# Optimization experiments

Hardware: AMD Instinct MI355X
Metric: run time of the kernel (lower is better)

Reference implementation:

```python
import jax, jax.numpy as jnp
import numpy as np

N_NODES = 100000


def _gcn_conv(x, edge_index, W, b, n_nodes):
    # GCNConv: add self-loops, symmetric degree normalization, then
    # out[dst] += norm * (x @ W)[src], plus bias.
    src, dst = edge_index[0], edge_index[1]
    loops = jnp.arange(n_nodes, dtype=src.dtype)
    src = jnp.concatenate([src, loops])
    dst = jnp.concatenate([dst, loops])
    deg = jax.ops.segment_sum(jnp.ones_like(dst, dtype=x.dtype), dst,
                              num_segments=n_nodes)
    dinv = jnp.where(deg > 0, jax.lax.rsqrt(deg), 0.0)
    norm = dinv[src] * dinv[dst]            # [E+N]
    h = x @ W                               # [N, out]  (transform BEFORE gather)
    msg = h[src] * norm[:, None]            # [E+N, out]
    out = jax.ops.segment_sum(msg, dst, num_segments=n_nodes)
    return out + b


def setup_inputs() -> dict:
    key = jax.random.key(0)
    ks = jax.random.split(key, 5)
    x = jax.random.normal(ks[0], (N_NODES, 512), dtype=jnp.float32)
    edge_index = jax.random.randint(ks[1], (2, 3200000), 0, N_NODES, dtype=jnp.int64)
    W1 = jax.random.normal(ks[2], (512, 16), dtype=jnp.float32) * (1.0 / np.sqrt(512))
    b1 = jnp.zeros((16,), dtype=jnp.float32)
    W2 = jax.random.normal(ks[3], (16, 7), dtype=jnp.float32) * (1.0 / np.sqrt(16))
    b2 = jnp.zeros((7,), dtype=jnp.float32)
    return {"x": x, "edge_index": edge_index, "W1": W1, "b1": b1, "W2": W2, "b2": b2}


def reference(x, edge_index, W1, b1, W2, b2):
    n = x.shape[0]
    h = _gcn_conv(x, edge_index, W1, b1, n)
    h = jax.nn.relu(h)
    # F.dropout(training=False) is identity in eval mode
    h = _gcn_conv(h, edge_index, W2, b2, n)
    return jax.nn.log_softmax(h, axis=1)
```

## Files before the change

### kernel.cpp

```cpp
#include <hip/hip_runtime.h>
#include <hip/hip_bf16.h>

#define N_NODES 100000
#define N_EDGES 3200000
#define F_IN    512
#define F_H     16
#define F_OUT   7
#define NB      391
#define GPART   512
#define PER_BLK 6256
#define NTILES  6250
#define CAPB    10240

typedef unsigned int u32;
typedef __attribute__((ext_vector_type(8))) __bf16 bf16x8;
typedef __attribute__((ext_vector_type(4))) float f32x4;

union FragU { uint4 q; bf16x8 v; };

static __device__ __forceinline__ float bflo(u32 u) { return __uint_as_float(u << 16); }
static __device__ __forceinline__ float bfhi(u32 u) { return __uint_as_float(u & 0xFFFF0000u); }
static __device__ __forceinline__ unsigned short f2bf(float f) {
  u32 x = __float_as_uint(f);
  x += 0x7FFF + ((x >> 16) & 1);
  return (unsigned short)(x >> 16);
}
static __device__ __forceinline__ u32 cvt2(float a, float b) {
  u32 r;
  asm("v_cvt_pk_bf16_f32 %0, %1, %2" : "=v"(r) : "v"(a), "v"(b));
  return r;
}

__global__ __launch_bounds__(256) void k_hist(const int* __restrict__ dst,
                                              int* __restrict__ hist,
                                              int* __restrict__ bcnt) {
  __shared__ int h[NB];
  int tid = threadIdx.x, blk = blockIdx.x;
  for (int b = tid; b < NB; b += 256) h[b] = 0;
  __syncthreads();
  int e0 = blk * PER_BLK;
  int n = min(PER_BLK, N_EDGES - e0);
  const int4* d4 = (const int4*)(dst + e0);
  for (int i = tid; i < (n >> 2); i += 256) {
    int4 d = d4[i];
    atomicAdd(&h[d.x >> 8], 1);
    atomicAdd(&h[d.y >> 8], 1);
    atomicAdd(&h[d.z >> 8], 1);
    atomicAdd(&h[d.w >> 8], 1);
  }
  __syncthreads();
  for (int b = tid; b < NB; b += 256) {
    int c = h[b];
    hist[blk * NB + b] = c;
    if (c) atomicAdd(&bcnt[b], c);
  }
}

__global__ __launch_bounds__(512) void k_scanprep(const int* __restrict__ bcnt,
                                                  int* __restrict__ pbase,
                                                  int* __restrict__ gcur,
                                                  const float* __restrict__ W1,
                                                  uint4* __restrict__ bfragG) {
  int tid = threadIdx.x;
  if (blockIdx.x == 1) {
    for (int idx = tid; idx < 1024; idx += 512) {
      int kk = idx >> 6, lane = idx & 63;
      int col = lane & 15, g = lane >> 4;
      int k0 = kk * 32 + g * 8;
      uint4 q;
      q.x = cvt2(W1[(k0 + 0) * 16 + col], W1[(k0 + 1) * 16 + col]);
      q.y = cvt2(W1[(k0 + 2) * 16 + col], W1[(k0 + 3) * 16 + col]);
      q.z = cvt2(W1[(k0 + 4) * 16 + col], W1[(k0 + 5) * 16 + col]);
      q.w = cvt2(W1[(k0 + 6) * 16 + col], W1[(k0 + 7) * 16 + col]);
      bfragG[idx] = q;
    }
    return;
  }
  __shared__ int lds[512];
  int c = (tid < NB) ? bcnt[tid] : 0;
  lds[tid] = c;
  __syncthreads();
  for (int off = 1; off < 512; off <<= 1) {
    int v = (tid >= off) ? lds[tid - off] : 0;
    __syncthreads();
    lds[tid] += v;
    __syncthreads();
  }
  int ex = lds[tid] - c;
  if (tid <= NB) pbase[tid] = ex;
  if (tid < NB) gcur[tid] = ex;
}

__global__ __launch_bounds__(256) void k_part(const int* __restrict__ src,
                                              const int* __restrict__ dst,
                                              const int* __restrict__ hist,
                                              int* __restrict__ gcur,
                                              u32* __restrict__ pairs) {
  __shared__ int lbase[NB];
  __shared__ int lcur[NB];
  int tid = threadIdx.x, blk = blockIdx.x;
  for (int b = tid; b < NB; b += 256) {
    int c = hist[blk * NB + b];
    lbase[b] = c ? atomicAdd(&gcur[b], c) : 0;
    lcur[b] = 0;
  }
  __syncthreads();
  int e0 = blk * PER_BLK;
  int n = min(PER_BLK, N_EDGES - e0);
  const int4* s4 = (const int4*)(src + e0);
  const int4* d4 = (const int4*)(dst + e0);
  for (int i = tid; i < (n >> 2); i += 256) {
    int4 sv = s4[i];
    int4 dv = d4[i];
    { int b = dv.x >> 8; u32 v = ((u32)(dv.x & 255) << 17) | (u32)sv.x;
      pairs[lbase[b] + atomicAdd(&lcur[b], 1)] = v; }
    { int b = dv.y >> 8; u32 v = ((u32)(dv.y & 255) << 17) | (u32)sv.y;
      pairs[lbase[b] + atomicAdd(&lcur[b], 1)] = v; }
    { int b = dv.z >> 8; u32 v = ((u32)(dv.z & 255) << 17) | (u32)sv.z;
      pairs[lbase[b] + atomicAdd(&lcur[b], 1)] = v; }
    { int b = dv.w >> 8; u32 v = ((u32)(dv.w & 255) << 17) | (u32)sv.w;
      pairs[lbase[b] + atomicAdd(&lcur[b], 1)] = v; }
  }
}

__global__ __launch_bounds__(256) void k_deg(const u32* __restrict__ pairs,
                                             const int* __restrict__ pbase,
                                             int* __restrict__ deg) {
  __shared__ int h[256];
  int tid = threadIdx.x, b = blockIdx.x;
  h[tid] = 0;
  __syncthreads();
  int base = pbase[b], cnt = pbase[b + 1] - base;
  for (int k = tid; k < cnt; k += 256)
    atomicAdd(&h[pairs[base + k] >> 17], 1);
  __syncthreads();
  int node = b * 256 + tid;
  if (node < N_NODES) deg[node] = h[tid];
}

__global__ __launch_bounds__(256) void k_gemm1(const float* __restrict__ x,
                                               const uint4* __restrict__ bfragG,
                                               const int* __restrict__ deg,
                                               unsigned short* __restrict__ h1p) {
  __shared__ __align__(16) char ldsbuf[2][64 * 80];
  int tid = threadIdx.x;
  int blockRow0 = blockIdx.x * 64;

  int r0 = tid >> 3, r1 = r0 + 32, s = tid & 7;
  bool ok1 = (blockRow0 + r1) < N_NODES;
  const float* x0 = x + (size_t)(blockRow0 + r0) * F_IN + s * 4;
  const float* x1 = x + (size_t)(blockRow0 + r1) * F_IN + s * 4;

  int wv = tid >> 6, lane = tid & 63;
  int col = lane & 15, g = lane >> 4;
  int wid = blockIdx.x * 4 + wv;
  int fragRow = wv * 16 + col;

  f32x4 acc = {0.f, 0.f, 0.f, 0.f};

  {
    float4 fA = *(const float4*)(x0);
    float4 fB = ok1 ? *(const float4*)(x1) : make_float4(0.f, 0.f, 0.f, 0.f);
    uint2 qA = {cvt2(fA.x, fA.y), cvt2(fA.z, fA.w)};
    uint2 qB = {cvt2(fB.x, fB.y), cvt2(fB.z, fB.w)};
    *(uint2*)(&ldsbuf[0][r0 * 80 + s * 8]) = qA;
    *(uint2*)(&ldsbuf[0][r1 * 80 + s * 8]) = qB;
  }
  __syncthreads();

#pragma unroll
  for (int kk = 0; kk < 16; kk++) {
    int cur = kk & 1;
    float4 fA, fB;
    if (kk < 15) {
      fA = *(const float4*)(x0 + (kk + 1) * 32);
      fB = ok1 ? *(const float4*)(x1 + (kk + 1) * 32) : make_float4(0.f, 0.f, 0.f, 0.f);
    }
    FragU a, b;
    a.q = *(const uint4*)(&ldsbuf[cur][fragRow * 80 + g * 16]);
    b.q = bfragG[kk * 64 + lane];
    acc = __builtin_amdgcn_mfma_f32_16x16x32_bf16(a.v, b.v, acc, 0, 0, 0);
    if (kk < 15) {
      uint2 qA = {cvt2(fA.x, fA.y), cvt2(fA.z, fA.w)};
      uint2 qB = {cvt2(fB.x, fB.y), cvt2(fB.z, fB.w)};
      *(uint2*)(&ldsbuf[cur ^ 1][r0 * 80 + s * 8]) = qA;
      *(uint2*)(&ldsbuf[cur ^ 1][r1 * 80 + s * 8]) = qB;
    }
    __syncthreads();
  }

#pragma unroll
  for (int r = 0; r < 4; r++) {
    int node = wid * 16 + g * 4 + r;
    if (node < N_NODES) {
      float di = rsqrtf((float)(deg[node] + 1));
      h1p[(size_t)node * F_H + col] = f2bf(di * acc[r]);
    }
  }
}

__global__ __launch_bounds__(512) void k_agg1(const u32* __restrict__ pairs,
                                              const int* __restrict__ pbase,
                                              const unsigned short* __restrict__ h1p,
                                              const float* __restrict__ b1,
                                              const float* __restrict__ W2,
                                              unsigned short* __restrict__ gfp) {
  __shared__ u32 col[CAPB];
  __shared__ int hist256[256];
  __shared__ int scan_[256];
  __shared__ int excl[256];
  __shared__ int cur[256];
  int tid = threadIdx.x, b = blockIdx.x;
  if (tid < 256) { hist256[tid] = 0; cur[tid] = 0; }
  __syncthreads();
  int base = pbase[b], cnt = pbase[b + 1] - base;
  for (int k = tid; k < cnt; k += 512)
    atomicAdd(&hist256[pairs[base + k] >> 17], 1);
  __syncthreads();
  if (tid < 256) scan_[tid] = hist256[tid];
  __syncthreads();
  for (int off = 1; off < 256; off <<= 1) {
    int v = 0;
    if (tid < 256 && tid >= off) v = scan_[tid - off];
    __syncthreads();
    if (tid < 256) scan_[tid] += v;
    __syncthreads();
  }
  if (tid < 256) excl[tid] = scan_[tid] - hist256[tid];
  __syncthreads();
  for (int k = tid; k < cnt; k += 512) {
    u32 v = pairs[base + k];
    int dl = v >> 17;
    col[excl[dl] + atomicAdd(&cur[dl], 1)] = v & 0x1FFFF;
  }
  __syncthreads();

  int dl = tid >> 1, h = tid & 1;
  int node = b * 256 + dl;
  if (node >= N_NODES) return;
  int s0 = excl[dl], c0 = hist256[dl];
  const uint4* hp = (const uint4*)h1p;
  float a[8] = {0.f, 0.f, 0.f, 0.f, 0.f, 0.f, 0.f, 0.f};
  for (int e = s0; e < s0 + c0; e++) {
    uint4 hv = hp[col[e] * 2 + h];
    a[0] += bflo(hv.x); a[1] += bfhi(hv.x);
    a[2] += bflo(hv.y); a[3] += bfhi(hv.y);
    a[4] += bflo(hv.z); a[5] += bfhi(hv.z);
    a[6] += bflo(hv.w); a[7] += bfhi(hv.w);
  }
  {
    uint4 hv = hp[node * 2 + h];
    a[0] += bflo(hv.x); a[1] += bfhi(hv.x);
    a[2] += bflo(hv.y); a[3] += bfhi(hv.y);
    a[4] += bflo(hv.z); a[5] += bfhi(hv.z);
    a[6] += bflo(hv.w); a[7] += bfhi(hv.w);
  }
  float di = rsqrtf((float)(c0 + 1));
  float own[8];
#pragma unroll
  for (int k = 0; k < 8; k++)
    own[k] = fmaxf(di * a[k] + b1[h * 8 + k], 0.f);
  float oth[8];
#pragma unroll
  for (int k = 0; k < 8; k++) oth[k] = __shfl_xor(own[k], 1, 64);
  if (h == 0) {
    float o[7] = {0.f, 0.f, 0.f, 0.f, 0.f, 0.f, 0.f};
#pragma unroll
    for (int k = 0; k < 8; k++)
#pragma unroll
      for (int j = 0; j < 7; j++)
        o[j] += own[k] * W2[k * 7 + j] + oth[k] * W2[(k + 8) * 7 + j];
    uint4 q;
    q.x = cvt2(di * o[0], di * o[1]);
    q.y = cvt2(di * o[2], di * o[3]);
    q.z = cvt2(di * o[4], di * o[5]);
    q.w = cvt2(di * o[6], 0.f);
    ((uint4*)gfp)[node] = q;
  }
}

__global__ __launch_bounds__(512) void k_agg2(const u32* __restrict__ pairs,
                                              const int* __restrict__ pbase,
                                              const unsigned short* __restrict__ gfp,
                                              const float* __restrict__ b2,
                                              float* __restrict__ out) {
  __shared__ u32 col[CAPB];
  __shared__ int hist256[256];
  __shared__ int scan_[256];
  __shared__ int excl[256];
  __shared__ int cur[256];
  int tid = threadIdx.x, b = blockIdx.x;
  if (tid < 256) { hist256[tid] = 0; cur[tid] = 0; }
  __syncthreads();
  int base = pbase[b], cnt = pbase[b + 1] - base;
  for (int k = tid; k < cnt; k += 512)
    atomicAdd(&hist256[pairs[base + k] >> 17], 1);
  __syncthreads();
  if (tid < 256) scan_[tid] = hist256[tid];
  __syncthreads();
  for (int off = 1; off < 256; off <<= 1) {
    int v = 0;
    if (tid < 256 && tid >= off) v = scan_[tid - off];
    __syncthreads();
    if (tid < 256) scan_[tid] += v;
    __syncthreads();
  }
  if (tid < 256) excl[tid] = scan_[tid] - hist256[tid];
  __syncthreads();
  for (int k = tid; k < cnt; k += 512) {
    u32 v = pairs[base + k];
    int dl = v >> 17;
    col[excl[dl] + atomicAdd(&cur[dl], 1)] = v & 0x1FFFF;
  }
  __syncthreads();

  int dl = tid >> 1, h = tid & 1;
  int node = b * 256 + dl;
  if (node >= N_NODES) return;
  int s0 = excl[dl], c0 = hist256[dl];
  const uint4* gp = (const uint4*)gfp;
  float a[7] = {0.f, 0.f, 0.f, 0.f, 0.f, 0.f, 0.f};
  for (int e = s0 + h; e < s0 + c0; e += 2) {
    uint4 gv = gp[col[e]];
    a[0] += bflo(gv.x); a[1] += bfhi(gv.x);
    a[2] += bflo(gv.y); a[3] += bfhi(gv.y);
    a[4] += bflo(gv.z); a[5] += bfhi(gv.z);
    a[6] += bflo(gv.w);
  }
#pragma unroll
  for (int j = 0; j < 7; j++) a[j] += __shfl_xor(a[j], 1, 64);
  if (h == 0) {
    uint4 sv = gp[node];
    a[0] += bflo(sv.x); a[1] += bfhi(sv.x);
    a[2] += bflo(sv.y); a[3] += bfhi(sv.y);
    a[4] += bflo(sv.z); a[5] += bfhi(sv.z);
    a[6] += bflo(sv.w);
    float di = rsqrtf((float)(c0 + 1));
    float v[7];
#pragma unroll
    for (int j = 0; j < 7; j++) v[j] = di * a[j] + b2[j];
    float m = v[0];
#pragma unroll
    for (int j = 1; j < 7; j++) m = fmaxf(m, v[j]);
    float s = 0.f;
#pragma unroll
    for (int j = 0; j < 7; j++) s += __expf(v[j] - m);
    float ls = m + logf(s);
#pragma unroll
    for (int j = 0; j < 7; j++) out[(size_t)node * 7 + j] = v[j] - ls;
  }
}

extern "C" void kernel_launch(void* const* d_in, const int* in_sizes, int n_in,
                              void* d_out, int out_size, void* d_ws, size_t ws_size,
                              hipStream_t stream) {
  const float* x  = (const float*)d_in[0];
  const int*   ei = (const int*)d_in[1];
  const float* W1 = (const float*)d_in[2];
  const float* b1 = (const float*)d_in[3];
  const float* W2 = (const float*)d_in[4];
  const float* b2 = (const float*)d_in[5];
  float* out = (float*)d_out;

  char* base = (char*)d_ws;
  int*   bcnt   = (int*)(base + 0);
  int*   deg    = (int*)(base + 2048);
  int*   pbase  = (int*)(base + 402176);
  int*   gcur   = (int*)(base + 404224);
  uint4* bfragG = (uint4*)(base + 406272);
  int*   hist   = (int*)(base + 422656);
  u32*   pairs  = (u32*)(base + 1223424);
  unsigned short* h1p = (unsigned short*)(base + 14023424);
  unsigned short* gfp = (unsigned short*)(base + 17223424);

  hipMemsetAsync(bcnt, 0, 2048, stream);

  k_hist    <<<GPART, 256, 0, stream>>>(ei + N_EDGES, hist, bcnt);
  k_scanprep<<<2, 512, 0, stream>>>(bcnt, pbase, gcur, W1, bfragG);
  k_part    <<<GPART, 256, 0, stream>>>(ei, ei + N_EDGES, hist, gcur, pairs);
  k_deg     <<<NB, 256, 0, stream>>>(pairs, pbase, deg);
  k_gemm1   <<<(NTILES + 3) / 4, 256, 0, stream>>>(x, bfragG, deg, h1p);
  k_agg1    <<<NB, 512, 0, stream>>>(pairs, pbase, h1p, b1, W2, gfp);
  k_agg2    <<<NB, 512, 0, stream>>>(pairs, pbase, gfp, b2, out);
}
```

Baseline: 167.5 us.

## Use fixed-capacity edge buckets and precompute per-node offsets once

```diff
diff --git a/kernel.cpp b/kernel.cpp
--- a/kernel.cpp
+++ b/kernel.cpp
@@ -11,6 +11,7 @@
 #define PER_BLK 6256
 #define NTILES  6250
 #define CAPB    10240
+#define NPAD    (NB * 256)
 
 typedef unsigned int u32;
 typedef __attribute__((ext_vector_type(8))) __bf16 bf16x8;
@@ -31,15 +32,37 @@
   return r;
 }
 
-__global__ __launch_bounds__(256) void k_hist(const int* __restrict__ dst,
-                                              int* __restrict__ hist,
-                                              int* __restrict__ bcnt) {
+__global__ __launch_bounds__(512) void k_prep(int* __restrict__ gcur,
+                                              const float* __restrict__ W1,
+                                              uint4* __restrict__ bfragG) {
+  int tid = threadIdx.x;
+  if (tid < NB) gcur[tid] = tid * CAPB;
+  for (int idx = tid; idx < 1024; idx += 512) {
+    int kk = idx >> 6, lane = idx & 63;
+    int col = lane & 15, g = lane >> 4;
+    int k0 = kk * 32 + g * 8;
+    uint4 q;
+    q.x = cvt2(W1[(k0 + 0) * 16 + col], W1[(k0 + 1) * 16 + col]);
+    q.y = cvt2(W1[(k0 + 2) * 16 + col], W1[(k0 + 3) * 16 + col]);
+    q.z = cvt2(W1[(k0 + 4) * 16 + col], W1[(k0 + 5) * 16 + col]);
+    q.w = cvt2(W1[(k0 + 6) * 16 + col], W1[(k0 + 7) * 16 + col]);
+    bfragG[idx] = q;
+  }
+}
+
+__global__ __launch_bounds__(256) void k_part(const int* __restrict__ src,
+                                              const int* __restrict__ dst,
+                                              int* __restrict__ gcur,
+                                              u32* __restrict__ pairs) {
   __shared__ int h[NB];
+  __shared__ int lbase[NB];
+  __shared__ int lcur[NB];
   int tid = threadIdx.x, blk = blockIdx.x;
   for (int b = tid; b < NB; b += 256) h[b] = 0;
   __syncthreads();
   int e0 = blk * PER_BLK;
   int n = min(PER_BLK, N_EDGES - e0);
+  const int4* s4 = (const int4*)(src + e0);
   const int4* d4 = (const int4*)(dst + e0);
   for (int i = tid; i < (n >> 2); i += 256) {
     int4 d = d4[i];
@@ -51,64 +74,10 @@
   __syncthreads();
   for (int b = tid; b < NB; b += 256) {
     int c = h[b];
-    hist[blk * NB + b] = c;
-    if (c) atomicAdd(&bcnt[b], c);
-  }
-}
-
-__global__ __launch_bounds__(512) void k_scanprep(const int* __restrict__ bcnt,
-                                                  int* __restrict__ pbase,
-                                                  int* __restrict__ gcur,
-                                                  const float* __restrict__ W1,
-                                                  uint4* __restrict__ bfragG) {
-  int tid = threadIdx.x;
-  if (blockIdx.x == 1) {
-    for (int idx = tid; idx < 1024; idx += 512) {
-      int kk = idx >> 6, lane = idx & 63;
-      int col = lane & 15, g = lane >> 4;
-      int k0 = kk * 32 + g * 8;
-      uint4 q;
-      q.x = cvt2(W1[(k0 + 0) * 16 + col], W1[(k0 + 1) * 16 + col]);
-      q.y = cvt2(W1[(k0 + 2) * 16 + col], W1[(k0 + 3) * 16 + col]);
-      q.z = cvt2(W1[(k0 + 4) * 16 + col], W1[(k0 + 5) * 16 + col]);
-      q.w = cvt2(W1[(k0 + 6) * 16 + col], W1[(k0 + 7) * 16 + col]);
-      bfragG[idx] = q;
-    }
-    return;
-  }
-  __shared__ int lds[512];
-  int c = (tid < NB) ? bcnt[tid] : 0;
-  lds[tid] = c;
-  __syncthreads();
-  for (int off = 1; off < 512; off <<= 1) {
-    int v = (tid >= off) ? lds[tid - off] : 0;
-    __syncthreads();
-    lds[tid] += v;
-    __syncthreads();
-  }
-  int ex = lds[tid] - c;
-  if (tid <= NB) pbase[tid] = ex;
-  if (tid < NB) gcur[tid] = ex;
-}
-
-__global__ __launch_bounds__(256) void k_part(const int* __restrict__ src,
-                                              const int* __restrict__ dst,
-                                              const int* __restrict__ hist,
-                                              int* __restrict__ gcur,
-                                              u32* __restrict__ pairs) {
-  __shared__ int lbase[NB];
-  __shared__ int lcur[NB];
-  int tid = threadIdx.x, blk = blockIdx.x;
-  for (int b = tid; b < NB; b += 256) {
-    int c = hist[blk * NB + b];
     lbase[b] = c ? atomicAdd(&gcur[b], c) : 0;
     lcur[b] = 0;
   }
   __syncthreads();
-  int e0 = blk * PER_BLK;
-  int n = min(PER_BLK, N_EDGES - e0);
-  const int4* s4 = (const int4*)(src + e0);
-  const int4* d4 = (const int4*)(dst + e0);
   for (int i = tid; i < (n >> 2); i += 256) {
     int4 sv = s4[i];
     int4 dv = d4[i];
@@ -124,23 +93,36 @@
 }
 
 __global__ __launch_bounds__(256) void k_deg(const u32* __restrict__ pairs,
-                                             const int* __restrict__ pbase,
-                                             int* __restrict__ deg) {
+                                             const int* __restrict__ gcur,
+                                             int* __restrict__ dega,
+                                             int* __restrict__ excla) {
   __shared__ int h[256];
+  __shared__ int sc[256];
   int tid = threadIdx.x, b = blockIdx.x;
   h[tid] = 0;
   __syncthreads();
-  int base = pbase[b], cnt = pbase[b + 1] - base;
+  int base = b * CAPB;
+  int cnt = gcur[b] - base;
   for (int k = tid; k < cnt; k += 256)
     atomicAdd(&h[pairs[base + k] >> 17], 1);
   __syncthreads();
+  int c = h[tid];
+  sc[tid] = c;
+  __syncthreads();
+  for (int off = 1; off < 256; off <<= 1) {
+    int v = (tid >= off) ? sc[tid - off] : 0;
+    __syncthreads();
+    sc[tid] += v;
+    __syncthreads();
+  }
   int node = b * 256 + tid;
-  if (node < N_NODES) deg[node] = h[tid];
+  dega[node] = c;
+  excla[node] = sc[tid] - c;
 }
 
 __global__ __launch_bounds__(256) void k_gemm1(const float* __restrict__ x,
                                                const uint4* __restrict__ bfragG,
-                                               const int* __restrict__ deg,
+                                               const int* __restrict__ dega,
                                                unsigned short* __restrict__ h1p) {
   __shared__ __align__(16) char ldsbuf[2][64 * 80];
   int tid = threadIdx.x;
@@ -193,52 +175,45 @@
   for (int r = 0; r < 4; r++) {
     int node = wid * 16 + g * 4 + r;
     if (node < N_NODES) {
-      float di = rsqrtf((float)(deg[node] + 1));
+      float di = rsqrtf((float)(dega[node] + 1));
       h1p[(size_t)node * F_H + col] = f2bf(di * acc[r]);
     }
   }
 }
 
 __global__ __launch_bounds__(512) void k_agg1(const u32* __restrict__ pairs,
-                                              const int* __restrict__ pbase,
+                                              const int* __restrict__ gcur,
+                                              const int* __restrict__ dega,
+                                              const int* __restrict__ excla,
                                               const unsigned short* __restrict__ h1p,
                                               const float* __restrict__ b1,
                                               const float* __restrict__ W2,
                                               unsigned short* __restrict__ gfp) {
   __shared__ u32 col[CAPB];
-  __shared__ int hist256[256];
-  __shared__ int scan_[256];
-  __shared__ int excl[256];
+  __shared__ int exc[256];
+  __shared__ int dg[256];
   __shared__ int cur[256];
   int tid = threadIdx.x, b = blockIdx.x;
-  if (tid < 256) { hist256[tid] = 0; cur[tid] = 0; }
-  __syncthreads();
-  int base = pbase[b], cnt = pbase[b + 1] - base;
-  for (int k = tid; k < cnt; k += 512)
-    atomicAdd(&hist256[pairs[base + k] >> 17], 1);
-  __syncthreads();
-  if (tid < 256) scan_[tid] = hist256[tid];
-  __syncthreads();
-  for (int off = 1; off < 256; off <<= 1) {
-    int v = 0;
-    if (tid < 256 && tid >= off) v = scan_[tid - off];
-    __syncthreads();
-    if (tid < 256) scan_[tid] += v;
-    __syncthreads();
-  }
-  if (tid < 256) excl[tid] = scan_[tid] - hist256[tid];
-  __syncthreads();
+  if (tid < 256) {
+    int node = b * 256 + tid;
+    dg[tid] = dega[node];
+    exc[tid] = excla[node];
+    cur[tid] = 0;
+  }
+  __syncthreads();
+  int base = b * CAPB;
+  int cnt = gcur[b] - base;
   for (int k = tid; k < cnt; k += 512) {
     u32 v = pairs[base + k];
     int dl = v >> 17;
-    col[excl[dl] + atomicAdd(&cur[dl], 1)] = v & 0x1FFFF;
+    col[exc[dl] + atomicAdd(&cur[dl], 1)] = v & 0x1FFFF;
   }
   __syncthreads();
 
   int dl = tid >> 1, h = tid & 1;
   int node = b * 256 + dl;
   if (node >= N_NODES) return;
-  int s0 = excl[dl], c0 = hist256[dl];
+  int s0 = exc[dl], c0 = dg[dl];
   const uint4* hp = (const uint4*)h1p;
   float a[8] = {0.f, 0.f, 0.f, 0.f, 0.f, 0.f, 0.f, 0.f};
   for (int e = s0; e < s0 + c0; e++) {
@@ -280,44 +255,37 @@
 }
 
 __global__ __launch_bounds__(512) void k_agg2(const u32* __restrict__ pairs,
-                                              const int* __restrict__ pbase,
+                                              const int* __restrict__ gcur,
+                                              const int* __restrict__ dega,
+                                              const int* __restrict__ excla,
                                               const unsigned short* __restrict__ gfp,
                                               const float* __restrict__ b2,
                                               float* __restrict__ out) {
   __shared__ u32 col[CAPB];
-  __shared__ int hist256[256];
-  __shared__ int scan_[256];
-  __shared__ int excl[256];
+  __shared__ int exc[256];
+  __shared__ int dg[256];
   __shared__ int cur[256];
   int tid = threadIdx.x, b = blockIdx.x;
-  if (tid < 256) { hist256[tid] = 0; cur[tid] = 0; }
-  __syncthreads();
-  int base = pbase[b], cnt = pbase[b + 1] - base;
-  for (int k = tid; k < cnt; k += 512)
-    atomicAdd(&hist256[pairs[base + k] >> 17], 1);
-  __syncthreads();
-  if (tid < 256) scan_[tid] = hist256[tid];
-  __syncthreads();
-  for (int off = 1; off < 256; off <<= 1) {
-    int v = 0;
-    if (tid < 256 && tid >= off) v = scan_[tid - off];
-    __syncthreads();
-    if (tid < 256) scan_[tid] += v;
-    __syncthreads();
-  }
-  if (tid < 256) excl[tid] = scan_[tid] - hist256[tid];
-  __syncthreads();
+  if (tid < 256) {
+    int node = b * 256 + tid;
+    dg[tid] = dega[node];
+    exc[tid] = excla[node];
+    cur[tid] = 0;
+  }
+  __syncthreads();
+  int base = b * CAPB;
+  int cnt = gcur[b] - base;
   for (int k = tid; k < cnt; k += 512) {
     u32 v = pairs[base + k];
     int dl = v >> 17;
-    col[excl[dl] + atomicAdd(&cur[dl], 1)] = v & 0x1FFFF;
+    col[exc[dl] + atomicAdd(&cur[dl], 1)] = v & 0x1FFFF;
   }
   __syncthreads();
 
   int dl = tid >> 1, h = tid & 1;
   int node = b * 256 + dl;
   if (node >= N_NODES) return;
-  int s0 = excl[dl], c0 = hist256[dl];
+  int s0 = exc[dl], c0 = dg[dl];
   const uint4* gp = (const uint4*)gfp;
   float a[7] = {0.f, 0.f, 0.f, 0.f, 0.f, 0.f, 0.f};
   for (int e = s0 + h; e < s0 + c0; e += 2) {
@@ -363,23 +331,18 @@
   float* out = (float*)d_out;
 
   char* base = (char*)d_ws;
-  int*   bcnt   = (int*)(base + 0);
-  int*   deg    = (int*)(base + 2048);
-  int*   pbase  = (int*)(base + 402176);
-  int*   gcur   = (int*)(base + 404224);
-  uint4* bfragG = (uint4*)(base + 406272);
-  int*   hist   = (int*)(base + 422656);
-  u32*   pairs  = (u32*)(base + 1223424);
-  unsigned short* h1p = (unsigned short*)(base + 14023424);
-  unsigned short* gfp = (unsigned short*)(base + 17223424);
-
-  hipMemsetAsync(bcnt, 0, 2048, stream);
-
-  k_hist    <<<GPART, 256, 0, stream>>>(ei + N_EDGES, hist, bcnt);
-  k_scanprep<<<2, 512, 0, stream>>>(bcnt, pbase, gcur, W1, bfragG);
-  k_part    <<<GPART, 256, 0, stream>>>(ei, ei + N_EDGES, hist, gcur, pairs);
-  k_deg     <<<NB, 256, 0, stream>>>(pairs, pbase, deg);
-  k_gemm1   <<<(NTILES + 3) / 4, 256, 0, stream>>>(x, bfragG, deg, h1p);
-  k_agg1    <<<NB, 512, 0, stream>>>(pairs, pbase, h1p, b1, W2, gfp);
-  k_agg2    <<<NB, 512, 0, stream>>>(pairs, pbase, gfp, b2, out);
-}
+  int*   gcur   = (int*)(base + 0);
+  uint4* bfragG = (uint4*)(base + 2048);
+  int*   dega   = (int*)(base + 18432);
+  int*   excla  = (int*)(base + 418816);
+  u32*   pairs  = (u32*)(base + 819200);
+  unsigned short* h1p = (unsigned short*)(base + 16834560);
+  unsigned short* gfp = (unsigned short*)(base + 20034560);
+
+  k_prep <<<1, 512, 0, stream>>>(gcur, W1, bfragG);
+  k_part <<<GPART, 256, 0, stream>>>(ei, ei + N_EDGES, gcur, pairs);
+  k_deg  <<<NB, 256, 0, stream>>>(pairs, gcur, dega, excla);
+  k_gemm1<<<(NTILES + 3) / 4, 256, 0, stream>>>(x, bfragG, dega, h1p);
+  k_agg1 <<<NB, 512, 0, stream>>>(pairs, gcur, dega, excla, h1p, b1, W2, gfp);
+  k_agg2 <<<NB, 512, 0, stream>>>(pairs, gcur, dega, excla, gfp, b2, out);
+}
```

New measurement: 137.7 us. 1.22x faster.
